# Kernel tuning notes

Measured on AMD Instinct MI355X. Metric: run time of the kernel, lower is better.

The kernel has to match this reference:

```python
import jax, jax.numpy as jnp
import numpy as np

N = 100000      # nodes
E = 1600000     # edges (avg degree 16)
DIN = 128
DOUT = 128


def setup_inputs() -> dict:
    key = jax.random.key(0)
    k1, k2, k3, k4 = jax.random.split(key, 4)
    x = jax.random.normal(k1, (N, DIN), dtype=jnp.float32)
    edge_index = jax.random.randint(k2, (2, E), 0, N, dtype=jnp.int64)
    # guarantee every node appears at least once as a source row so that
    # degree > 0 everywhere (1/sqrt(0) would be inf, as in the torch code)
    row = edge_index[0].at[:N].set(jnp.arange(N, dtype=jnp.int64))
    edge_index = jnp.stack([row, edge_index[1]])
    W = jax.random.normal(k3, (DOUT, DIN), dtype=jnp.float32) / np.sqrt(DIN)
    b = jax.random.normal(k4, (DOUT,), dtype=jnp.float32) * 0.01
    return {"x": x, "edge_index": edge_index, "W": W, "b": b}


def reference(x, edge_index, W, b):
    # Math identical to: A = dense(add_self_loops(edge_index));
    # D = 1/sqrt(degree(edge_index[0]))  (degree WITHOUT self-loops);
    # out = (D_i * A_ij * D_j) @ (x W^T + b)
    row, col = edge_index[0], edge_index[1]
    deg = jax.ops.segment_sum(jnp.ones(row.shape[0], x.dtype), row, num_segments=N)
    d = jax.lax.rsqrt(deg)                      # [N]
    h = x @ W.T + b                             # [N, DOUT]
    # edge contributions: out[r] += D[r] * D[c] * h[c]  (duplicate edges sum, as to_dense does)
    agg = jax.ops.segment_sum(d[col][:, None] * h[col], row, num_segments=N)
    # self-loop term added for every node: D[i]^2 * h[i]
    out = d[:, None] * agg + (d * d)[:, None] * h
    return out
```

## Files before the change

### kernel.cpp

```cpp
#include <hip/hip_runtime.h>

#define D 128
#define BROWS 512
#define LOGB 9
#define NBMAX 256
#define CAP 9216
#define CHUNK 4096

typedef __attribute__((ext_vector_type(8))) short bf16x8;
typedef __attribute__((ext_vector_type(4))) float f32x4;

__device__ inline unsigned short f2bf(float f) {
    unsigned u = __float_as_uint(f);
    u += 0x7FFFu + ((u >> 16) & 1u);
    return (unsigned short)(u >> 16);
}
__device__ inline float bf2f(unsigned short h) {
    return __uint_as_float((unsigned)h << 16);
}
__device__ inline float bflo(unsigned u) { return __uint_as_float(u << 16); }
__device__ inline float bfhi(unsigned u) { return __uint_as_float(u & 0xFFFF0000u); }

__global__ __launch_bounds__(512) void k_bin(const int* __restrict__ row,
                                             const int* __restrict__ col,
                                             int E, int* __restrict__ gcur,
                                             unsigned* __restrict__ ebuf,
                                             const float* __restrict__ W,
                                             unsigned short* __restrict__ Wbh,
                                             unsigned short* __restrict__ Wbl) {
    __shared__ int lhist[NBMAX];
    __shared__ int sc[NBMAX];
    __shared__ int gbase[NBMAX];
    __shared__ unsigned sstage[CHUNK];
    __shared__ int sdest[CHUNK];
    int t = threadIdx.x;
    if (blockIdx.x < 8) {
        int base = blockIdx.x * 2048 + t;
        #pragma unroll
        for (int i = 0; i < 4; ++i) {
            int idx = base + i * 512;
            float wv = W[idx];
            unsigned short h = f2bf(wv);
            Wbh[idx] = h;
            Wbl[idx] = f2bf(wv - bf2f(h));
        }
    }
    int base = blockIdx.x * CHUNK;
    if (t < NBMAX) lhist[t] = 0;
    __syncthreads();
    int b[8], p[8]; unsigned pk[8];
    #pragma unroll
    for (int i = 0; i < 8; ++i) {
        int idx = base + i * 512 + t;
        if (idx < E) {
            int r = row[idx], c = col[idx];
            b[i] = r >> LOGB;
            pk[i] = ((unsigned)(r & (BROWS - 1)) << 17) | (unsigned)c;
            p[i] = atomicAdd(&lhist[b[i]], 1);
        } else b[i] = -1;
    }
    __syncthreads();
    if (t < 64) {
        int a0 = lhist[4*t], a1 = lhist[4*t+1], a2 = lhist[4*t+2], a3 = lhist[4*t+3];
        int s = a0 + a1 + a2 + a3;
        int incl = s;
        #pragma unroll
        for (int m = 1; m < 64; m <<= 1) {
            int tmp = __shfl_up(incl, m);
            if (t >= m) incl += tmp;
        }
        int excl = incl - s;
        sc[4*t] = excl; sc[4*t+1] = excl + a0;
        sc[4*t+2] = excl + a0 + a1; sc[4*t+3] = excl + a0 + a1 + a2;
        if (a0 > 0) gbase[4*t]   = atomicAdd(&gcur[4*t],   a0);
        if (a1 > 0) gbase[4*t+1] = atomicAdd(&gcur[4*t+1], a1);
        if (a2 > 0) gbase[4*t+2] = atomicAdd(&gcur[4*t+2], a2);
        if (a3 > 0) gbase[4*t+3] = atomicAdd(&gcur[4*t+3], a3);
    }
    __syncthreads();
    #pragma unroll
    for (int i = 0; i < 8; ++i) {
        if (b[i] >= 0) {
            int lidx = sc[b[i]] + p[i];
            int rel = gbase[b[i]] + p[i];
            sstage[lidx] = pk[i];
            sdest[lidx] = (rel < CAP) ? (b[i] * CAP + rel) : -1;
        }
    }
    __syncthreads();
    int total = sc[NBMAX - 1] + lhist[NBMAX - 1];
    for (int i = t; i < total; i += 512) {
        int d = sdest[i];
        if (d >= 0) ebuf[d] = sstage[i];
    }
}

__global__ __launch_bounds__(1024) void k_group(const int* __restrict__ gcur,
                                                const unsigned* __restrict__ ebuf,
                                                const float* __restrict__ x,
                                                int N, int NBK,
                                                float* __restrict__ dvals,
                                                int* __restrict__ rptr,
                                                int* __restrict__ csr_col,
                                                unsigned short* __restrict__ xs) {
    __shared__ unsigned sebuf[CAP];
    __shared__ int lhist[BROWS];
    __shared__ float sdl[BROWS];
    __shared__ int wtot[8];
    __shared__ int woff[8];
    __shared__ int sebase;
    int bkt = blockIdx.x, t = threadIdx.x;
    int cnt = gcur[bkt]; if (cnt > CAP) cnt = CAP;
    if (t < 64) {
        int acc = 0;
        for (int i = t; i < bkt; i += 64) {
            int g = gcur[i];
            acc += (g > CAP) ? CAP : g;
        }
        #pragma unroll
        for (int m = 1; m < 64; m <<= 1) acc += __shfl_xor(acc, m);
        if (t == 0) sebase = acc;
    }
    if (t < BROWS) lhist[t] = 0;
    __syncthreads();
    const unsigned* ep = ebuf + (size_t)bkt * CAP;
    for (int i = t; i < cnt; i += 1024) {
        unsigned e = ep[i];
        sebuf[i] = e;
        atomicAdd(&lhist[e >> 17], 1);
    }
    __syncthreads();
    int lane = t & 63, wv = t >> 6;
    int v = 0, incl = 0;
    if (t < BROWS) {
        v = lhist[t];
        incl = v;
        #pragma unroll
        for (int m = 1; m < 64; m <<= 1) {
            int tmp = __shfl_up(incl, m);
            if (lane >= m) incl += tmp;
        }
        if (lane == 63) wtot[wv] = incl;
    }
    __syncthreads();
    if (t < 8) {
        int w = wtot[t];
        int wincl = w;
        #pragma unroll
        for (int m = 1; m < 8; m <<= 1) {
            int tmp = __shfl_up(wincl, m);
            if (t >= m) wincl += tmp;
        }
        woff[t] = wincl - w;
    }
    __syncthreads();
    int ebase = sebase;
    if (t < BROWS) {
        int excl = woff[wv] + incl - v;
        int r = (bkt << LOGB) + t;
        float dl = rsqrtf((float)v);
        if (r < N) {
            rptr[r] = ebase + excl;
            dvals[r] = dl;
        }
        sdl[t] = dl;
        lhist[t] = excl;
    }
    if (bkt == NBK - 1 && t == 0) rptr[N] = ebase + cnt;
    if (bkt == 0 && t == 0) dvals[N] = 0.f;
    __syncthreads();
    for (int i = t; i < cnt; i += 1024) {
        unsigned e = sebuf[i];
        int rr = (int)(e >> 17);
        int p = atomicAdd(&lhist[rr], 1);
        csr_col[ebase + p] = (int)(e & 0x1FFFFu);
    }
    int rb = bkt << LOGB;
    const float4* x4 = (const float4*)x;
    for (int idx = t; idx < BROWS * 32; idx += 1024) {
        int rl = idx >> 5;
        int r = rb + rl;
        if (r < N) {
            float4 vv = x4[(size_t)r * 32 + (idx & 31)];
            float d = sdl[rl];
            ushort4 o = make_ushort4(f2bf(d * vv.x), f2bf(d * vv.y),
                                     f2bf(d * vv.z), f2bf(d * vv.w));
            ((ushort4*)xs)[(size_t)r * 32 + (idx & 31)] = o;
        }
    }
    if (bkt == 0 && t < 64)
        ((unsigned*)(xs + (size_t)N * D))[t] = 0u;
}

#define ACC8(v) do { \
    a[0] += bflo((v).x); a[1] += bfhi((v).x); \
    a[2] += bflo((v).y); a[3] += bfhi((v).y); \
    a[4] += bflo((v).z); a[5] += bfhi((v).z); \
    a[6] += bflo((v).w); a[7] += bfhi((v).w); } while (0)

__global__ __launch_bounds__(256) void k_rows(const unsigned short* __restrict__ xs,
                                              const int* __restrict__ rptr,
                                              const int* __restrict__ csr_col,
                                              const float* __restrict__ dvals,
                                              float* __restrict__ ssum,
                                              float* __restrict__ y, int N) {
    int wid = (blockIdx.x * blockDim.x + threadIdx.x) >> 6;
    if (wid >= N) return;
    int lane = threadIdx.x & 63;
    int grp = lane >> 4, sl = lane & 15;
    int s = rptr[wid];
    int n = rptr[wid + 1] - s;
    const uint4* xsv = (const uint4*)xs;

    int cc0 = csr_col[s + lane];
    int ccreg = (lane < n) ? cc0 : N;
    float sd = dvals[ccreg];
    uint4 vself = xsv[(size_t)wid * 16 + sl];

    float a[8] = {0.f, 0.f, 0.f, 0.f, 0.f, 0.f, 0.f, 0.f};
    int nf = (n < 64) ? n : 64;
    for (int k0 = 0; k0 < nf; k0 += 32) {
        int i0 = k0 + grp;
        int c0 = __shfl(ccreg, i0),      c1 = __shfl(ccreg, i0 + 4);
        int c2 = __shfl(ccreg, i0 + 8),  c3 = __shfl(ccreg, i0 + 12);
        int c4 = __shfl(ccreg, i0 + 16), c5 = __shfl(ccreg, i0 + 20);
        int c6 = __shfl(ccreg, i0 + 24), c7 = __shfl(ccreg, i0 + 28);
        uint4 v0 = xsv[(size_t)c0 * 16 + sl];
        uint4 v1 = xsv[(size_t)c1 * 16 + sl];
        uint4 v2 = xsv[(size_t)c2 * 16 + sl];
        uint4 v3 = xsv[(size_t)c3 * 16 + sl];
        uint4 v4 = xsv[(size_t)c4 * 16 + sl];
        uint4 v5 = xsv[(size_t)c5 * 16 + sl];
        uint4 v6 = xsv[(size_t)c6 * 16 + sl];
        uint4 v7 = xsv[(size_t)c7 * 16 + sl];
        __builtin_amdgcn_sched_barrier(0);
        ACC8(v0); ACC8(v1); ACC8(v2); ACC8(v3);
        ACC8(v4); ACC8(v5); ACC8(v6); ACC8(v7);
    }
    if (__builtin_expect(n > 64, 0)) {
        for (int idx = 64 + grp; idx < n; idx += 4) {
            int cc = csr_col[s + idx];
            uint4 v = xsv[(size_t)cc * 16 + sl];
            ACC8(v);
        }
        for (int idx = 64 + lane; idx < n; idx += 64)
            sd += dvals[csr_col[s + idx]];
    }
    if (grp == 0) ACC8(vself);

    #pragma unroll
    for (int j = 0; j < 8; ++j) {
        a[j] += __shfl_xor(a[j], 16);
        a[j] += __shfl_xor(a[j], 32);
    }
    #pragma unroll
    for (int m = 1; m < 64; m <<= 1) sd += __shfl_xor(sd, m);

    float dr = dvals[wid];
    if (grp < 2) {
        float4 o = (grp == 0) ? make_float4(a[0], a[1], a[2], a[3])
                              : make_float4(a[4], a[5], a[6], a[7]);
        o.x *= dr; o.y *= dr; o.z *= dr; o.w *= dr;
        ((float4*)(y + (size_t)wid * D))[sl * 2 + grp] = o;
    }
    if (lane == 0) ssum[wid] = dr * (dr + sd);
}

#define LDSW 136

__global__ __launch_bounds__(256, 2) void k_gemm(const unsigned short* __restrict__ Wbh,
                                                 const unsigned short* __restrict__ Wbl,
                                                 const float* __restrict__ b,
                                                 const float* __restrict__ ssum,
                                                 float* yo, int N) {
    __shared__ unsigned short Whi[128 * LDSW];
    __shared__ unsigned short Wlo[128 * LDSW];
    __shared__ float bs[D];
    int t = threadIdx.x;
    #pragma unroll
    for (int i = 0; i < 16; ++i) {
        int idx4 = i * 256 + t;
        int r = idx4 >> 5;
        int c = (idx4 & 31) * 4;
        ((ushort4*)&Whi[r * LDSW + c])[0] = ((const ushort4*)Wbh)[idx4];
        ((ushort4*)&Wlo[r * LDSW + c])[0] = ((const ushort4*)Wbl)[idx4];
    }
    if (t < D) bs[t] = b[t];
    __syncthreads();

    int wave = t >> 6, lane = t & 63;
    int quad = lane >> 4, mrow = lane & 15;
    int row_base = blockIdx.x * 128 + wave * 32;

    bf16x8 Ahi[2][4], Alo[2][4];
    #pragma unroll
    for (int s = 0; s < 2; ++s) {
        int grow = row_base + s * 16 + mrow;
        bool ok = grow < N;
        const float* yrow = yo + (size_t)(ok ? grow : 0) * D;
        #pragma unroll
        for (int kk = 0; kk < 4; ++kk) {
            int k0 = kk * 32 + quad * 8;
            float4 f0 = ok ? ((const float4*)(yrow + k0))[0] : make_float4(0, 0, 0, 0);
            float4 f1 = ok ? ((const float4*)(yrow + k0))[1] : make_float4(0, 0, 0, 0);
            float fv[8] = {f0.x, f0.y, f0.z, f0.w, f1.x, f1.y, f1.z, f1.w};
            #pragma unroll
            for (int j = 0; j < 8; ++j) {
                unsigned short h = f2bf(fv[j]);
                Ahi[s][kk][j] = (short)h;
                Alo[s][kk][j] = (short)f2bf(fv[j] - bf2f(h));
            }
        }
    }

    f32x4 acc[2][8];
    #pragma unroll
    for (int s = 0; s < 2; ++s)
        #pragma unroll
        for (int ct = 0; ct < 8; ++ct)
            acc[s][ct] = (f32x4){0.f, 0.f, 0.f, 0.f};

    #pragma unroll
    for (int ct = 0; ct < 8; ++ct) {
        int wrow = ct * 16 + mrow;
        #pragma unroll
        for (int kk = 0; kk < 4; ++kk) {
            int off = wrow * LDSW + kk * 32 + quad * 8;
            bf16x8 Bhi = *(const bf16x8*)&Whi[off];
            bf16x8 Blo = *(const bf16x8*)&Wlo[off];
            #pragma unroll
            for (int s = 0; s < 2; ++s) {
                acc[s][ct] = __builtin_amdgcn_mfma_f32_16x16x32_bf16(Ahi[s][kk], Bhi, acc[s][ct], 0, 0, 0);
                acc[s][ct] = __builtin_amdgcn_mfma_f32_16x16x32_bf16(Alo[s][kk], Bhi, acc[s][ct], 0, 0, 0);
                acc[s][ct] = __builtin_amdgcn_mfma_f32_16x16x32_bf16(Ahi[s][kk], Blo, acc[s][ct], 0, 0, 0);
            }
        }
    }

    #pragma unroll
    for (int s = 0; s < 2; ++s) {
        #pragma unroll
        for (int r = 0; r < 4; ++r) {
            int grow = row_base + s * 16 + quad * 4 + r;
            if (grow < N) {
                float sv = ssum[grow];
                #pragma unroll
                for (int ct = 0; ct < 8; ++ct) {
                    int col = ct * 16 + mrow;
                    yo[(size_t)grow * D + col] = acc[s][ct][r] + sv * bs[col];
                }
            }
        }
    }
}

extern "C" void kernel_launch(void* const* d_in, const int* in_sizes, int n_in,
                              void* d_out, int out_size, void* d_ws, size_t ws_size,
                              hipStream_t stream) {
    const float* x  = (const float*)d_in[0];
    const int*   ei = (const int*)d_in[1];
    const float* W  = (const float*)d_in[2];
    const float* b  = (const float*)d_in[3];
    float* out = (float*)d_out;
    int N = in_sizes[0] / D;
    int E = in_sizes[1] / 2;
    int NB = (N + BROWS - 1) / BROWS;
    int NCH = (E + CHUNK - 1) / CHUNK;

    int*            gcur    = (int*)d_ws;
    int*            rptr    = gcur + NBMAX;
    float*          dvals   = (float*)(rptr + N + 1);
    float*          ssum    = dvals + N + 1;
    int*            csr_col = (int*)(ssum + N);
    unsigned*       ebuf    = (unsigned*)(csr_col + E + 64);
    unsigned short* Wbh     = (unsigned short*)(ebuf + (size_t)NB * CAP);
    unsigned short* Wbl     = Wbh + D * D;
    uintptr_t xs_addr = (uintptr_t)(Wbl + D * D);
    xs_addr = (xs_addr + 15) & ~(uintptr_t)15;
    unsigned short* xs = (unsigned short*)xs_addr;

    hipMemsetAsync(gcur, 0, NBMAX * sizeof(int), stream);
    k_bin<<<NCH, 512, 0, stream>>>(ei, ei + E, E, gcur, ebuf, W, Wbh, Wbl);
    k_group<<<NB, 1024, 0, stream>>>(gcur, ebuf, x, N, NB, dvals, rptr, csr_col, xs);
    k_rows<<<(N + 3) / 4, 256, 0, stream>>>(xs, rptr, csr_col, dvals, ssum, out, N);
    k_gemm<<<(N + 127) / 128, 256, 0, stream>>>(Wbh, Wbl, b, ssum, out, N);
}
```

Before: 276.8 us.

## Process two CSR rows per wavefront in aggregation kernel with 16-edge steps

New measurement: 279.3 us. No clear change (+0.9%).

```diff
diff --git a/kernel.cpp b/kernel.cpp
--- a/kernel.cpp
+++ b/kernel.cpp
@@ -192,11 +192,11 @@
         ((unsigned*)(xs + (size_t)N * D))[t] = 0u;
 }
 
-#define ACC8(v) do { \
-    a[0] += bflo((v).x); a[1] += bfhi((v).x); \
-    a[2] += bflo((v).y); a[3] += bfhi((v).y); \
-    a[4] += bflo((v).z); a[5] += bfhi((v).z); \
-    a[6] += bflo((v).w); a[7] += bfhi((v).w); } while (0)
+#define ACC8(A, v) do { \
+    A[0] += bflo((v).x); A[1] += bfhi((v).x); \
+    A[2] += bflo((v).y); A[3] += bfhi((v).y); \
+    A[4] += bflo((v).z); A[5] += bfhi((v).z); \
+    A[6] += bflo((v).w); A[7] += bfhi((v).w); } while (0)
 
 __global__ __launch_bounds__(256) void k_rows(const unsigned short* __restrict__ xs,
                                               const int* __restrict__ rptr,
@@ -204,66 +204,108 @@
                                               const float* __restrict__ dvals,
                                               float* __restrict__ ssum,
                                               float* __restrict__ y, int N) {
-    int wid = (blockIdx.x * blockDim.x + threadIdx.x) >> 6;
-    if (wid >= N) return;
+    int wv = (blockIdx.x * blockDim.x + threadIdx.x) >> 6;
+    int r0 = wv * 2;
+    if (r0 >= N) return;
+    int r1 = r0 + 1;
+    bool has1 = (r1 < N);
     int lane = threadIdx.x & 63;
     int grp = lane >> 4, sl = lane & 15;
-    int s = rptr[wid];
-    int n = rptr[wid + 1] - s;
     const uint4* xsv = (const uint4*)xs;
 
-    int cc0 = csr_col[s + lane];
-    int ccreg = (lane < n) ? cc0 : N;
-    float sd = dvals[ccreg];
-    uint4 vself = xsv[(size_t)wid * 16 + sl];
-
-    float a[8] = {0.f, 0.f, 0.f, 0.f, 0.f, 0.f, 0.f, 0.f};
-    int nf = (n < 64) ? n : 64;
-    for (int k0 = 0; k0 < nf; k0 += 32) {
-        int i0 = k0 + grp;
-        int c0 = __shfl(ccreg, i0),      c1 = __shfl(ccreg, i0 + 4);
-        int c2 = __shfl(ccreg, i0 + 8),  c3 = __shfl(ccreg, i0 + 12);
-        int c4 = __shfl(ccreg, i0 + 16), c5 = __shfl(ccreg, i0 + 20);
-        int c6 = __shfl(ccreg, i0 + 24), c7 = __shfl(ccreg, i0 + 28);
-        uint4 v0 = xsv[(size_t)c0 * 16 + sl];
-        uint4 v1 = xsv[(size_t)c1 * 16 + sl];
-        uint4 v2 = xsv[(size_t)c2 * 16 + sl];
-        uint4 v3 = xsv[(size_t)c3 * 16 + sl];
-        uint4 v4 = xsv[(size_t)c4 * 16 + sl];
-        uint4 v5 = xsv[(size_t)c5 * 16 + sl];
-        uint4 v6 = xsv[(size_t)c6 * 16 + sl];
-        uint4 v7 = xsv[(size_t)c7 * 16 + sl];
+    int s0 = rptr[r0];
+    int n0 = rptr[r0 + 1] - s0;
+    int s1 = 0, n1 = 0;
+    if (has1) { s1 = rptr[r1]; n1 = rptr[r1 + 1] - s1; }
+
+    int cc0 = (lane < n0) ? csr_col[s0 + lane] : N;
+    int cc1 = (has1 && lane < n1) ? csr_col[s1 + lane] : N;
+    float sd0 = dvals[cc0];
+    float sd1 = dvals[cc1];
+    uint4 vs0 = xsv[(size_t)r0 * 16 + sl];
+    uint4 vs1 = xsv[(size_t)(has1 ? r1 : N) * 16 + sl];
+
+    float a0[8] = {0.f, 0.f, 0.f, 0.f, 0.f, 0.f, 0.f, 0.f};
+    float a1[8] = {0.f, 0.f, 0.f, 0.f, 0.f, 0.f, 0.f, 0.f};
+    int nf0 = (n0 < 64) ? n0 : 64;
+    int nf1 = (n1 < 64) ? n1 : 64;
+    int jm0 = (nf0 + 15) >> 4;
+    int jm1 = (nf1 + 15) >> 4;
+    if (!has1) jm1 = 0;
+    int jmax = (jm0 > jm1) ? jm0 : jm1;
+
+    for (int j = 0; j < jmax; ++j) {
+        int base = j * 16 + grp;
+        bool do0 = (j < jm0), do1 = (j < jm1);
+        uint4 u0, u1, u2, u3, w0, w1, w2, w3;
+        if (do0) {
+            int c0 = __shfl(cc0, base),      c1 = __shfl(cc0, base + 4);
+            int c2 = __shfl(cc0, base + 8),  c3 = __shfl(cc0, base + 12);
+            u0 = xsv[(size_t)c0 * 16 + sl];
+            u1 = xsv[(size_t)c1 * 16 + sl];
+            u2 = xsv[(size_t)c2 * 16 + sl];
+            u3 = xsv[(size_t)c3 * 16 + sl];
+        }
+        if (do1) {
+            int c0 = __shfl(cc1, base),      c1 = __shfl(cc1, base + 4);
+            int c2 = __shfl(cc1, base + 8),  c3 = __shfl(cc1, base + 12);
+            w0 = xsv[(size_t)c0 * 16 + sl];
+            w1 = xsv[(size_t)c1 * 16 + sl];
+            w2 = xsv[(size_t)c2 * 16 + sl];
+            w3 = xsv[(size_t)c3 * 16 + sl];
+        }
         __builtin_amdgcn_sched_barrier(0);
-        ACC8(v0); ACC8(v1); ACC8(v2); ACC8(v3);
-        ACC8(v4); ACC8(v5); ACC8(v6); ACC8(v7);
-    }
-    if (__builtin_expect(n > 64, 0)) {
-        for (int idx = 64 + grp; idx < n; idx += 4) {
-            int cc = csr_col[s + idx];
+        if (do0) { ACC8(a0, u0); ACC8(a0, u1); ACC8(a0, u2); ACC8(a0, u3); }
+        if (do1) { ACC8(a1, w0); ACC8(a1, w1); ACC8(a1, w2); ACC8(a1, w3); }
+    }
+    if (__builtin_expect(n0 > 64, 0)) {
+        for (int idx = 64 + grp; idx < n0; idx += 4) {
+            int cc = csr_col[s0 + idx];
             uint4 v = xsv[(size_t)cc * 16 + sl];
-            ACC8(v);
-        }
-        for (int idx = 64 + lane; idx < n; idx += 64)
-            sd += dvals[csr_col[s + idx]];
-    }
-    if (grp == 0) ACC8(vself);
-
-    #pragma unroll
-    for (int j = 0; j < 8; ++j) {
-        a[j] += __shfl_xor(a[j], 16);
-        a[j] += __shfl_xor(a[j], 32);
-    }
-    #pragma unroll
-    for (int m = 1; m < 64; m <<= 1) sd += __shfl_xor(sd, m);
-
-    float dr = dvals[wid];
+            ACC8(a0, v);
+        }
+        for (int idx = 64 + lane; idx < n0; idx += 64)
+            sd0 += dvals[csr_col[s0 + idx]];
+    }
+    if (__builtin_expect(n1 > 64, 0)) {
+        for (int idx = 64 + grp; idx < n1; idx += 4) {
+            int cc = csr_col[s1 + idx];
+            uint4 v = xsv[(size_t)cc * 16 + sl];
+            ACC8(a1, v);
+        }
+        for (int idx = 64 + lane; idx < n1; idx += 64)
+            sd1 += dvals[csr_col[s1 + idx]];
+    }
+    if (grp == 0) { ACC8(a0, vs0); ACC8(a1, vs1); }
+
+    #pragma unroll
+    for (int q = 0; q < 8; ++q) {
+        a0[q] += __shfl_xor(a0[q], 16);
+        a0[q] += __shfl_xor(a0[q], 32);
+        a1[q] += __shfl_xor(a1[q], 16);
+        a1[q] += __shfl_xor(a1[q], 32);
+    }
+    #pragma unroll
+    for (int m = 1; m < 64; m <<= 1) {
+        sd0 += __shfl_xor(sd0, m);
+        sd1 += __shfl_xor(sd1, m);
+    }
+
+    float dr0 = dvals[r0];
+    float dr1 = has1 ? dvals[r1] : 0.f;
     if (grp < 2) {
-        float4 o = (grp == 0) ? make_float4(a[0], a[1], a[2], a[3])
-                              : make_float4(a[4], a[5], a[6], a[7]);
-        o.x *= dr; o.y *= dr; o.z *= dr; o.w *= dr;
-        ((float4*)(y + (size_t)wid * D))[sl * 2 + grp] = o;
-    }
-    if (lane == 0) ssum[wid] = dr * (dr + sd);
+        float4 o = (grp == 0) ? make_float4(a0[0], a0[1], a0[2], a0[3])
+                              : make_float4(a0[4], a0[5], a0[6], a0[7]);
+        o.x *= dr0; o.y *= dr0; o.z *= dr0; o.w *= dr0;
+        ((float4*)(y + (size_t)r0 * D))[sl * 2 + grp] = o;
+    } else if (has1) {
+        float4 o = (grp == 2) ? make_float4(a1[0], a1[1], a1[2], a1[3])
+                              : make_float4(a1[4], a1[5], a1[6], a1[7]);
+        o.x *= dr1; o.y *= dr1; o.z *= dr1; o.w *= dr1;
+        ((float4*)(y + (size_t)r1 * D))[sl * 2 + (grp - 2)] = o;
+    }
+    if (lane == 0) ssum[r0] = dr0 * (dr0 + sd0);
+    if (lane == 32 && has1) ssum[r1] = dr1 * (dr1 + sd1);
 }
 
 #define LDSW 136
@@ -382,6 +424,6 @@
     hipMemsetAsync(gcur, 0, NBMAX * sizeof(int), stream);
     k_bin<<<NCH, 512, 0, stream>>>(ei, ei + E, E, gcur, ebuf, W, Wbh, Wbl);
     k_group<<<NB, 1024, 0, stream>>>(gcur, ebuf, x, N, NB, dvals, rptr, csr_col, xs);
-    k_rows<<<(N + 3) / 4, 256, 0, stream>>>(xs, rptr, csr_col, dvals, ssum, out, N);
+    k_rows<<<(N + 7) / 8, 256, 0, stream>>>(xs, rptr, csr_col, dvals, ssum, out, N);
     k_gemm<<<(N + 127) / 128, 256, 0, stream>>>(Wbh, Wbl, b, ssum, out, N);
 }
```
